# Performance work log

Hardware: AMD Instinct MI355X
Metric: run time of the kernel (lower is better)

## Reference

```python
import jax, jax.numpy as jnp
import numpy as np
from jax import lax

B, L, D, H = 2, 2048, 2048, 16
DH = D // H            # 128 head dim
D_REL = 64             # relevance projection dim (class const)
K = max(1, int(0.25 * L))  # top-K_FRAC tokens per query
NEG_INF = float('-inf')


def setup_inputs() -> dict:
    key = jax.random.key(0)
    ks = jax.random.split(key, 8)
    s = D ** (-0.5)
    return {
        'hidden_states': jax.random.normal(ks[0], (B, L, D), jnp.float32),
        'relevance':     jax.random.normal(ks[1], (B, L, D), jnp.float32),
        # torch nn.Linear weights are [out_features, in_features]
        'W_q_rel': jax.random.normal(ks[2], (D_REL, D), jnp.float32) * s,
        'W_k_rel': jax.random.normal(ks[3], (D_REL, D), jnp.float32) * s,
        'W_q': jax.random.normal(ks[4], (D, D), jnp.float32) * s,
        'W_k': jax.random.normal(ks[5], (D, D), jnp.float32) * s,
        'W_v': jax.random.normal(ks[6], (D, D), jnp.float32) * s,
        'W_o': jax.random.normal(ks[7], (D, D), jnp.float32) * s,
    }


def _rel_scores(relevance, W_q_rel, W_k_rel):
    # low-rank relevance logits, causally masked: [B, L, L]
    q = relevance @ W_q_rel.T   # [B, L, d_rel]
    k = relevance @ W_k_rel.T   # [B, L, d_rel]
    scores = jnp.einsum('bqd,bkd->bqk', q, k) * (D_REL ** -0.5)
    future = jnp.triu(jnp.ones((L, L), dtype=bool), k=1)
    return jnp.where(future[None], NEG_INF, scores)


def _sparse_mask(rel_scores):
    # additive mask [B, 1, L, L]: top-k per query row -> 0.0, else -inf; diag 0.0
    _, topk_idx = lax.top_k(rel_scores, K)            # [B, L, K]
    b = jnp.arange(B)[:, None, None]
    q = jnp.arange(L)[None, :, None]
    mask = jnp.full((B, L, L), NEG_INF, dtype=rel_scores.dtype)
    mask = mask.at[b, q, topk_idx].set(0.0)
    diag = jnp.arange(L)
    mask = mask.at[:, diag, diag].set(0.0)
    return mask[:, None]  # [B, 1, L, L]


def _attention(hidden_states, W_q, W_k, W_v, W_o, add_mask):
    # standard multi-head attention with additive mask (the wrapped frozen attn)
    q = (hidden_states @ W_q.T).reshape(B, L, H, DH)
    k = (hidden_states @ W_k.T).reshape(B, L, H, DH)
    v = (hidden_states @ W_v.T).reshape(B, L, H, DH)
    scores = jnp.einsum('bqhd,bkhd->bhqk', q, k) * (DH ** -0.5)
    scores = scores + add_mask                      # [B, H, L, L]
    p = jax.nn.softmax(scores, axis=-1)
    ctx = jnp.einsum('bhqk,bkhd->bqhd', p, v).reshape(B, L, D)
    return ctx @ W_o.T


def reference(hidden_states, relevance, W_q_rel, W_k_rel, W_q, W_k, W_v, W_o):
    # Phase 1 path (step >= SPARSE_FROM), no external attention_mask:
    # combined = causal(-inf upper-tri) + sparse top-k mask.
    rel = _rel_scores(relevance, W_q_rel, W_k_rel)
    sparse = _sparse_mask(rel)                      # [B, 1, L, L]
    future = jnp.triu(jnp.ones((L, L), dtype=bool), k=1)
    causal = jnp.where(future, NEG_INF, 0.0).astype(hidden_states.dtype)
    combined = causal[None, None] + sparse          # [B, 1, L, L]
    return _attention(hidden_states, W_q, W_k, W_v, W_o, combined)
```

## Files before the change

kernel.cpp:

```cpp
#include <hip/hip_runtime.h>
#include <math.h>
#include <stdint.h>

#define Bb 2
#define Lq 2048
#define Dm 2048
#define Hh 16
#define DH 128
#define DREL 64
#define KTOP 512

#define NEG_INF (-__builtin_huge_valf())

typedef __attribute__((ext_vector_type(8))) short bf16x8;
typedef __attribute__((ext_vector_type(4))) float f32x4;

static __device__ __forceinline__ unsigned short f2bf(float f) {
  unsigned int u = __float_as_uint(f);
  u += 0x7fffu + ((u >> 16) & 1u);
  return (unsigned short)(u >> 16);
}

static __device__ __forceinline__ void gload16(const void* g, void* lds) {
  __builtin_amdgcn_global_load_lds(
      (const __attribute__((address_space(1))) uint32_t*)(uintptr_t)g,
      (__attribute__((address_space(3))) uint32_t*)(uint32_t)(uintptr_t)lds,
      16, 0, 0);
}

__global__ __launch_bounds__(256) void conv_bf16(const float* __restrict__ in,
                                                 unsigned short* __restrict__ out,
                                                 int n8, float scale) {
  const int i = blockIdx.x * 256 + threadIdx.x;
  if (i >= n8) return;
  const float4 f0 = ((const float4*)in)[2 * i];
  const float4 f1 = ((const float4*)in)[2 * i + 1];
  bf16x8 o;
  o[0] = (short)f2bf(f0.x * scale); o[1] = (short)f2bf(f0.y * scale);
  o[2] = (short)f2bf(f0.z * scale); o[3] = (short)f2bf(f0.w * scale);
  o[4] = (short)f2bf(f1.x * scale); o[5] = (short)f2bf(f1.y * scale);
  o[6] = (short)f2bf(f1.z * scale); o[7] = (short)f2bf(f1.w * scale);
  *(bf16x8*)(out + 8 * (size_t)i) = o;
}

__global__ __launch_bounds__(256) void conv_bf16_w4(const float* __restrict__ w0,
                                                    const float* __restrict__ w1,
                                                    const float* __restrict__ w2,
                                                    const float* __restrict__ w3,
                                                    unsigned short* __restrict__ out,
                                                    float s0) {
  const int sel = blockIdx.y;
  const float* in = (sel == 0) ? w0 : (sel == 1) ? w1 : (sel == 2) ? w2 : w3;
  const float scale = (sel == 0) ? s0 : 1.0f;
  const int i = blockIdx.x * 256 + threadIdx.x;
  const float4 f0 = ((const float4*)in)[2 * i];
  const float4 f1 = ((const float4*)in)[2 * i + 1];
  bf16x8 o;
  o[0] = (short)f2bf(f0.x * scale); o[1] = (short)f2bf(f0.y * scale);
  o[2] = (short)f2bf(f0.z * scale); o[3] = (short)f2bf(f0.w * scale);
  o[4] = (short)f2bf(f1.x * scale); o[5] = (short)f2bf(f1.y * scale);
  o[6] = (short)f2bf(f1.z * scale); o[7] = (short)f2bf(f1.w * scale);
  *(bf16x8*)(out + (size_t)sel * Dm * Dm + 8 * (size_t)i) = o;
}

template <bool BF16OUT>
__global__ __launch_bounds__(512, 2) void gemm256(const unsigned short* __restrict__ A,
                                                  const unsigned short* __restrict__ W,
                                                  void* __restrict__ Cv,
                                                  int M, int N, int Kd) {
  __shared__ unsigned short As[2][2][128][64];
  __shared__ unsigned short Bs[2][2][128][64];

  const int tid = threadIdx.x;
  const int w = tid >> 6;
  const int lane = tid & 63;
  const int l15 = lane & 15;
  const int quad = lane >> 4;
  const int wm = w >> 2;
  const int wn = w & 3;

  const int gx = N >> 8;
  const int nwg = (M >> 8) * gx;
  const int cpx = nwg >> 3;
  const int bid = (int)blockIdx.x;
  const int lin = (bid & 7) * cpx + (bid >> 3);
  const int bx = lin % gx, by = lin / gx;
  const int m0 = by * 256, n0 = bx * 256;

  const int srow = lane >> 3;
  const int sslot = (lane & 7) ^ srow;
  const size_t rowK = (size_t)Kd;
  const unsigned short* aG0 = A + (size_t)(m0 + w * 8 + srow) * rowK + sslot * 8;
  const unsigned short* aG1 = aG0 + 64 * rowK;
  const unsigned short* aG2 = aG0 + 128 * rowK;
  const unsigned short* aG3 = aG0 + 192 * rowK;
  const unsigned short* bG0 = W + (size_t)(n0 + w * 8 + srow) * rowK + sslot * 8;
  const unsigned short* bG1 = bG0 + 64 * rowK;
  const unsigned short* bG2 = bG0 + 128 * rowK;
  const unsigned short* bG3 = bG0 + 192 * rowK;

  f32x4 acc[8][4];
#pragma unroll
  for (int i = 0; i < 8; ++i)
#pragma unroll
    for (int j = 0; j < 4; ++j) acc[i][j] = (f32x4){0.f, 0.f, 0.f, 0.f};

  bf16x8 af[4][2];
  bf16x8 bfr[2][2];
  const int swz = (l15 & 7) * 8;

#define STAGE(BUF, T)                                         \
  do {                                                        \
    const size_t ko = (size_t)(T) * 64;                       \
    gload16(aG0 + ko, &As[BUF][0][w * 8][0]);                 \
    gload16(aG1 + ko, &As[BUF][0][64 + w * 8][0]);            \
    gload16(aG2 + ko, &As[BUF][1][w * 8][0]);                 \
    gload16(aG3 + ko, &As[BUF][1][64 + w * 8][0]);            \
    gload16(bG0 + ko, &Bs[BUF][0][w * 8][0]);                 \
    gload16(bG1 + ko, &Bs[BUF][0][64 + w * 8][0]);            \
    gload16(bG2 + ko, &Bs[BUF][1][w * 8][0]);                 \
    gload16(bG3 + ko, &Bs[BUF][1][64 + w * 8][0]);            \
  } while (0)

#define LOAD_A(BUF, MH)                                                        \
  _Pragma("unroll") for (int mi = 0; mi < 4; ++mi)                             \
    _Pragma("unroll") for (int ks = 0; ks < 2; ++ks)                           \
      af[mi][ks] = *(const bf16x8*)&As[BUF][wm][(MH) * 64 + mi * 16 + l15]     \
                                      [(ks * 32 + quad * 8) ^ swz];

#define LOAD_B(BUF, NH)                                                        \
  _Pragma("unroll") for (int ni = 0; ni < 2; ++ni)                             \
    _Pragma("unroll") for (int ks = 0; ks < 2; ++ks)                           \
      bfr[ni][ks] = *(const bf16x8*)&Bs[BUF][wn >> 1]                          \
          [(wn & 1) * 64 + ((NH) * 2 + ni) * 16 + l15]                         \
          [(ks * 32 + quad * 8) ^ swz];

#define PHASE_MFMA(MH, NH)                                                     \
  do {                                                                         \
    __builtin_amdgcn_s_setprio(1);                                             \
    _Pragma("unroll") for (int mi = 0; mi < 4; ++mi)                           \
      _Pragma("unroll") for (int ni = 0; ni < 2; ++ni) {                       \
        acc[(MH) * 4 + mi][(NH) * 2 + ni] =                                    \
            __builtin_amdgcn_mfma_f32_16x16x32_bf16(                           \
                af[mi][0], bfr[ni][0], acc[(MH) * 4 + mi][(NH) * 2 + ni], 0, 0, 0); \
        acc[(MH) * 4 + mi][(NH) * 2 + ni] =                                    \
            __builtin_amdgcn_mfma_f32_16x16x32_bf16(                           \
                af[mi][1], bfr[ni][1], acc[(MH) * 4 + mi][(NH) * 2 + ni], 0, 0, 0); \
      }                                                                        \
    __builtin_amdgcn_s_setprio(0);                                             \
  } while (0)

  STAGE(0, 0);
  __syncthreads();

  const int nt = Kd >> 6;
  int buf = 0;
  for (int t = 0; t < nt; ++t) {
    if (t + 1 < nt) STAGE(buf ^ 1, t + 1);

    LOAD_A(buf, 0);
    LOAD_B(buf, 0);
    PHASE_MFMA(0, 0);
    __builtin_amdgcn_s_barrier();

    LOAD_B(buf, 1);
    PHASE_MFMA(0, 1);
    __builtin_amdgcn_s_barrier();

    LOAD_A(buf, 1);
    PHASE_MFMA(1, 1);
    __builtin_amdgcn_s_barrier();

    LOAD_B(buf, 0);
    PHASE_MFMA(1, 0);

    __syncthreads();
    buf ^= 1;
  }
#undef STAGE
#undef LOAD_A
#undef LOAD_B
#undef PHASE_MFMA

#pragma unroll
  for (int im = 0; im < 8; ++im) {
#pragma unroll
    for (int in = 0; in < 4; ++in) {
      const int col = n0 + wn * 64 + in * 16 + l15;
#pragma unroll
      for (int r = 0; r < 4; ++r) {
        const int row = m0 + wm * 128 + im * 16 + quad * 4 + r;
        if (BF16OUT)
          ((unsigned short*)Cv)[(size_t)row * N + col] = f2bf(acc[im][in][r]);
        else
          ((float*)Cv)[(size_t)row * N + col] = acc[im][in][r];
      }
    }
  }
}

#define RKS 8
__global__ __launch_bounds__(256) void relproj2(const float* __restrict__ A,
                                                const float* __restrict__ Wqr,
                                                const float* __restrict__ Wkr,
                                                float* __restrict__ partq,
                                                float* __restrict__ partk, int M) {
  const float* W = blockIdx.z ? Wkr : Wqr;
  float* part = blockIdx.z ? partk : partq;
  __shared__ float As[16][128];
  __shared__ float Bs[16][64];
  const int ks = blockIdx.x;
  const int m0 = blockIdx.y * 128;
  const int tid = threadIdx.x;
  const int tx = tid & 15;
  const int ty = tid >> 4;
  const int lr = tid >> 1, lk = (tid & 1) * 8;
  const int wr = tid >> 2, wk = (tid & 3) * 4;

  float acc[8][4];
#pragma unroll
  for (int i = 0; i < 8; ++i)
#pragma unroll
    for (int j = 0; j < 4; ++j) acc[i][j] = 0.f;

  const int k00 = ks * (Dm / RKS);
  for (int k0 = k00; k0 < k00 + Dm / RKS; k0 += 16) {
    {
      const float* ap = A + (size_t)(m0 + lr) * Dm + k0 + lk;
      float4 a0 = *(const float4*)(ap);
      float4 a1 = *(const float4*)(ap + 4);
      As[lk + 0][lr] = a0.x; As[lk + 1][lr] = a0.y;
      As[lk + 2][lr] = a0.z; As[lk + 3][lr] = a0.w;
      As[lk + 4][lr] = a1.x; As[lk + 5][lr] = a1.y;
      As[lk + 6][lr] = a1.z; As[lk + 7][lr] = a1.w;
    }
    {
      const float* bp = W + (size_t)wr * Dm + k0 + wk;
      float4 b0 = *(const float4*)(bp);
      Bs[wk + 0][wr] = b0.x; Bs[wk + 1][wr] = b0.y;
      Bs[wk + 2][wr] = b0.z; Bs[wk + 3][wr] = b0.w;
    }
    __syncthreads();
#pragma unroll
    for (int kk = 0; kk < 16; ++kk) {
      float af[8], bf[4];
#pragma unroll
      for (int i = 0; i < 8; ++i) af[i] = As[kk][ty * 8 + i];
#pragma unroll
      for (int j = 0; j < 4; ++j) bf[j] = Bs[kk][tx * 4 + j];
#pragma unroll
      for (int i = 0; i < 8; ++i)
#pragma unroll
        for (int j = 0; j < 4; ++j) acc[i][j] += af[i] * bf[j];
    }
    __syncthreads();
  }

#pragma unroll
  for (int i = 0; i < 8; ++i) {
    float* pp = part + ((size_t)ks * M + m0 + ty * 8 + i) * DREL + tx * 4;
    *(float4*)pp = make_float4(acc[i][0], acc[i][1], acc[i][2], acc[i][3]);
  }
}

__global__ __launch_bounds__(256) void relreduce(const float* __restrict__ pq,
                                                 const float* __restrict__ pk,
                                                 float* __restrict__ qrel,
                                                 float* __restrict__ krel, int n4) {
  const int i = blockIdx.x * 256 + threadIdx.x;
  if (i >= n4) return;
  float4 sq = make_float4(0, 0, 0, 0), sk = sq;
  for (int s = 0; s < RKS; ++s) {
    float4 a = ((const float4*)pq)[(size_t)s * n4 + i];
    float4 b = ((const float4*)pk)[(size_t)s * n4 + i];
    sq.x += a.x; sq.y += a.y; sq.z += a.z; sq.w += a.w;
    sk.x += b.x; sk.y += b.y; sk.z += b.z; sk.w += b.w;
  }
  ((float4*)qrel)[i] = sq;
  ((float4*)krel)[i] = sk;
}

__global__ __launch_bounds__(256) void relscore(const float* __restrict__ qrel,
                                                const float* __restrict__ krel,
                                                float* __restrict__ S) {
  const int jt = blockIdx.x, qt = blockIdx.y, b = blockIdx.z;
  if (jt > qt) return;
  __shared__ float As[16][128];
  __shared__ float Bs[16][128];
  const int tid = threadIdx.x;
  const int q0 = qt * 128, j0 = jt * 128;
  const int tx = tid & 15, ty = tid >> 4;
  const int lr = tid >> 1, lk = (tid & 1) * 8;
  const float* Ab = qrel + (size_t)b * Lq * DREL;
  const float* Kb = krel + (size_t)b * Lq * DREL;

  float acc[8][8];
#pragma unroll
  for (int i = 0; i < 8; ++i)
#pragma unroll
    for (int j = 0; j < 8; ++j) acc[i][j] = 0.f;

  for (int k0 = 0; k0 < DREL; k0 += 16) {
    {
      const float* ap = Ab + (size_t)(q0 + lr) * DREL + k0 + lk;
      float4 a0 = *(const float4*)(ap);
      float4 a1 = *(const float4*)(ap + 4);
      As[lk + 0][lr] = a0.x; As[lk + 1][lr] = a0.y;
      As[lk + 2][lr] = a0.z; As[lk + 3][lr] = a0.w;
      As[lk + 4][lr] = a1.x; As[lk + 5][lr] = a1.y;
      As[lk + 6][lr] = a1.z; As[lk + 7][lr] = a1.w;
    }
    {
      const float* bp = Kb + (size_t)(j0 + lr) * DREL + k0 + lk;
      float4 b0 = *(const float4*)(bp);
      float4 b1 = *(const float4*)(bp + 4);
      Bs[lk + 0][lr] = b0.x; Bs[lk + 1][lr] = b0.y;
      Bs[lk + 2][lr] = b0.z; Bs[lk + 3][lr] = b0.w;
      Bs[lk + 4][lr] = b1.x; Bs[lk + 5][lr] = b1.y;
      Bs[lk + 6][lr] = b1.z; Bs[lk + 7][lr] = b1.w;
    }
    __syncthreads();
#pragma unroll
    for (int kk = 0; kk < 16; ++kk) {
      float af[8], bf[8];
#pragma unroll
      for (int i = 0; i < 8; ++i) af[i] = As[kk][ty * 8 + i];
#pragma unroll
      for (int j = 0; j < 8; ++j) bf[j] = Bs[kk][tx * 8 + j];
#pragma unroll
      for (int i = 0; i < 8; ++i)
#pragma unroll
        for (int j = 0; j < 8; ++j) acc[i][j] += af[i] * bf[j];
    }
    __syncthreads();
  }

  const float sc = 0.125f;
#pragma unroll
  for (int i = 0; i < 8; ++i) {
    float* cp = S + ((size_t)b * Lq + q0 + ty * 8 + i) * Lq + j0 + tx * 8;
    ((float4*)cp)[0] = make_float4(acc[i][0] * sc, acc[i][1] * sc, acc[i][2] * sc, acc[i][3] * sc);
    ((float4*)cp)[1] = make_float4(acc[i][4] * sc, acc[i][5] * sc, acc[i][6] * sc, acc[i][7] * sc);
  }
}

__global__ __launch_bounds__(256) void relselect(const float* __restrict__ S,
                                                 uint32_t* __restrict__ mask) {
  const int w = threadIdx.x >> 6;
  const int lane = threadIdx.x & 63;
  const int ridx = blockIdx.x * 4 + w;
  const int qi = ridx & (Lq - 1);
  const int n = qi + 1;
  const float* srow = S + (size_t)ridx * Lq;

  uint32_t keys[32];
#pragma unroll
  for (int t = 0; t < 32; ++t) {
    const int j = t * 64 + lane;
    const uint32_t u = __float_as_uint(srow[j]);
    const uint32_t k = (u & 0x80000000u) ? ~u : (u | 0x80000000u);
    keys[t] = (j < n) ? k : 0u;
  }

  uint32_t kth = 0u;
  if (n > KTOP) {
    uint32_t pref = 0u;
    int rem = KTOP;
    for (int bit = 31; bit >= 0; --bit) {
      const uint32_t cand = pref | (1u << bit);
      const uint32_t lim = 1u << bit;
      int c = 0;
#pragma unroll
      for (int t = 0; t < 32; ++t) c += ((keys[t] ^ cand) < lim) ? 1 : 0;
      c += __shfl_xor(c, 1);
      c += __shfl_xor(c, 2);
      c += __shfl_xor(c, 4);
      c += __shfl_xor(c, 8);
      c += __shfl_xor(c, 16);
      c += __shfl_xor(c, 32);
      if (c >= rem) pref = cand;
      else rem -= c;
    }
    kth = pref;
  }

  uint32_t* mrow = mask + (size_t)ridx * (Lq / 32);
#pragma unroll
  for (int t = 0; t < 32; ++t) {
    const int j = t * 64 + lane;
    const bool ok = (j < n) && (keys[t] >= kth || j == qi);
    const unsigned long long bal = __ballot(ok);
    if (lane == 0) {
      mrow[2 * t] = (uint32_t)bal;
      mrow[2 * t + 1] = (uint32_t)(bal >> 32);
    }
  }
}

#define ATQ 128
#define TK 64
__global__ __launch_bounds__(512, 4) void attn_flash3(const unsigned short* __restrict__ qkv,
                                                      const uint32_t* __restrict__ mask,
                                                      unsigned short* __restrict__ ctx) {
  __shared__ unsigned short Ks[2][TK][136];
  __shared__ unsigned short Vt[2][2][64][72];
  __shared__ uint32_t mw[2][ATQ][2];

  const int qt = (blockIdx.z == 0) ? ((Lq / ATQ) - 1 - (int)blockIdx.x) : (int)blockIdx.x;
  const int h = blockIdx.y;
  const int b = blockIdx.z;
  const int tid = threadIdx.x;
  const int w = tid >> 6;
  const int lane = tid & 63;
  const int l15 = lane & 15;
  const int quad = lane >> 4;
  const int q0 = qt * ATQ;
  const int STR = 3 * Dm;

  const unsigned short* kbp = qkv + 2048;
  const unsigned short* vbp = qkv + 4096;

  const int myq = q0 + w * 16 + l15;
  const unsigned short* qrow = qkv + (size_t)(b * Lq + myq) * STR + h * DH;
  bf16x8 bq[4];
#pragma unroll
  for (int kk = 0; kk < 4; ++kk) bq[kk] = *(const bf16x8*)(qrow + kk * 32 + quad * 8);

  f32x4 O[8];
#pragma unroll
  for (int f = 0; f < 8; ++f) O[f] = (f32x4){0.f, 0.f, 0.f, 0.f};
  float l_lane = 0.f;

  const int nt = (q0 + ATQ) / TK;

  const int skey = (tid & 255) >> 2;
  const int scg  = tid & 3;
  const int mq   = (tid & 255) >> 1;
  const int msel = tid & 1;
  const int tv = tid - 256;
  const int vkp = tv & 31;
  const int vdg = (tv >> 5) & 7;
  const int vhalf = vkp >> 4;
  const int vkp16 = vkp & 15;
  const int dwc = ((vkp16 >> 1) & 3) * 4 + (vkp16 >> 3) * 2 + (vkp16 & 1);

  const uint32_t* mrow_base = mask + (size_t)(b * Lq + q0 + mq) * (Lq / 32) + msel;
  const unsigned short* krow_base = kbp + (size_t)(b * Lq + skey) * STR + h * DH + scg * 32;
  const unsigned short* vrow_base = vbp + (size_t)(b * Lq + 2 * vkp) * STR + h * DH + vdg * 16;

  bf16x8 r0, r1, r2, r3;
  uint32_t mreg = 0;

#define LOADREGS(KT)                                                       \
  do {                                                                     \
    const int kbase_ = (KT) * TK;                                          \
    if (tid < 256) {                                                       \
      const unsigned short* kr = krow_base + (size_t)kbase_ * STR;         \
      r0 = *(const bf16x8*)(kr);                                           \
      r1 = *(const bf16x8*)(kr + 8);                                       \
      r2 = *(const bf16x8*)(kr + 16);                                      \
      r3 = *(const bf16x8*)(kr + 24);                                      \
      mreg = mrow_base[(KT) * 2];                                          \
    } else {                                                               \
      const unsigned short* vr = vrow_base + (size_t)kbase_ * STR;         \
      r0 = *(const bf16x8*)(vr);                                           \
      r1 = *(const bf16x8*)(vr + 8);                                       \
      r2 = *(const bf16x8*)(vr + STR);                                     \
      r3 = *(const bf16x8*)(vr + STR + 8);                                 \
    }                                                                      \
  } while (0)

#define WRITELDS(BUF)                                                      \
  do {                                                                     \
    if (tid < 256) {                                                       \
      *(bf16x8*)&Ks[BUF][skey][scg * 32 + 0]  = r0;                        \
      *(bf16x8*)&Ks[BUF][skey][scg * 32 + 8]  = r1;                        \
      *(bf16x8*)&Ks[BUF][skey][scg * 32 + 16] = r2;                        \
      *(bf16x8*)&Ks[BUF][skey][scg * 32 + 24] = r3;                        \
      mw[BUF][mq][msel] = mreg;                                            \
    } else {                                                               \
      _Pragma("unroll") for (int i = 0; i < 8; ++i) {                      \
        const int d = vdg * 16 + i;                                        \
        const uint32_t pk = (uint32_t)(unsigned short)r0[i] |              \
                            ((uint32_t)(unsigned short)r2[i] << 16);       \
        ((uint32_t*)&Vt[BUF][vhalf][d >> 1][0])[(d & 1) * 16 + dwc] = pk;  \
      }                                                                    \
      _Pragma("unroll") for (int i = 0; i < 8; ++i) {                      \
        const int d = vdg * 16 + 8 + i;                                    \
        const uint32_t pk = (uint32_t)(unsigned short)r1[i] |              \
                            ((uint32_t)(unsigned short)r3[i] << 16);       \
        ((uint32_t*)&Vt[BUF][vhalf][d >> 1][0])[(d & 1) * 16 + dwc] = pk;  \
      }                                                                    \
    }                                                                      \
  } while (0)

  LOADREGS(0);
  WRITELDS(0);
  __syncthreads();

  int buf = 0;
  for (int kt = 0; kt < nt; ++kt) {
    const bool more = (kt + 1 < nt);
    if (more) LOADREGS(kt + 1);

    __builtin_amdgcn_s_setprio(1);
#pragma unroll
    for (int hh = 0; hh < 2; ++hh) {
      f32x4 acc0 = (f32x4){0.f, 0.f, 0.f, 0.f};
      f32x4 acc1 = acc0;
#pragma unroll
      for (int kk = 0; kk < 4; ++kk) {
        bf16x8 a0 = *(const bf16x8*)&Ks[buf][hh * 32 + l15][kk * 32 + quad * 8];
        bf16x8 a1 = *(const bf16x8*)&Ks[buf][hh * 32 + 16 + l15][kk * 32 + quad * 8];
        acc0 = __builtin_amdgcn_mfma_f32_16x16x32_bf16(a0, bq[kk], acc0, 0, 0, 0);
        acc1 = __builtin_amdgcn_mfma_f32_16x16x32_bf16(a1, bq[kk], acc1, 0, 0, 0);
      }

      const uint32_t mword = mw[buf][w * 16 + l15][hh];
      bf16x8 bp;
      float ps = 0.f;
#pragma unroll
      for (int r = 0; r < 4; ++r) {
        const float p0 = ((mword >> (quad * 4 + r)) & 1u) ? __builtin_amdgcn_exp2f(acc0[r]) : 0.f;
        const float p1 = ((mword >> (16 + quad * 4 + r)) & 1u) ? __builtin_amdgcn_exp2f(acc1[r]) : 0.f;
        ps += p0 + p1;
        bp[r] = (short)f2bf(p0);
        bp[4 + r] = (short)f2bf(p1);
      }
      l_lane += ps;

#pragma unroll
      for (int f = 0; f < 8; ++f) {
        const int d = f * 16 + l15;
        bf16x8 av = *(const bf16x8*)&Vt[buf][hh][d >> 1][(d & 1) * 32 + quad * 8];
        O[f] = __builtin_amdgcn_mfma_f32_16x16x32_bf16(av, bp, O[f], 0, 0, 0);
      }
    }
    __builtin_amdgcn_s_setprio(0);

    if (more) WRITELDS(buf ^ 1);
    __syncthreads();
    buf ^= 1;
  }
#undef LOADREGS
#undef WRITELDS

  l_lane += __shfl_xor(l_lane, 16);
  l_lane += __shfl_xor(l_lane, 32);
  const float rl = 1.0f / l_lane;

  unsigned short* orow = ctx + ((size_t)(b * Lq + q0 + w * 16 + l15)) * Dm + h * DH;
#pragma unroll
  for (int f = 0; f < 8; ++f) {
    ushort4 o4;
    o4.x = f2bf(O[f][0] * rl);
    o4.y = f2bf(O[f][1] * rl);
    o4.z = f2bf(O[f][2] * rl);
    o4.w = f2bf(O[f][3] * rl);
    *(ushort4*)(orow + f * 16 + quad * 4) = o4;
  }
}

extern "C" void kernel_launch(void* const* d_in, const int* in_sizes, int n_in,
                              void* d_out, int out_size, void* d_ws, size_t ws_size,
                              hipStream_t stream) {
  const float* hs  = (const float*)d_in[0];
  const float* rel = (const float*)d_in[1];
  const float* Wqr = (const float*)d_in[2];
  const float* Wkr = (const float*)d_in[3];
  const float* Wq  = (const float*)d_in[4];
  const float* Wk  = (const float*)d_in[5];
  const float* Wv  = (const float*)d_in[6];
  const float* Wo  = (const float*)d_in[7];
  float* out = (float*)d_out;

  const int M = Bb * Lq;
  const int ND = Dm * Dm;
  char* ws = (char*)d_ws;
  size_t off = 0;
  float* qrel = (float*)(ws + off); off += (size_t)M * DREL * 4;
  float* krel = (float*)(ws + off); off += (size_t)M * DREL * 4;
  uint32_t* maskb = (uint32_t*)(ws + off); off += (size_t)M * (Lq / 32) * 4;
  float* partq = (float*)(ws + off); off += (size_t)RKS * M * DREL * 4;
  float* partk = (float*)(ws + off); off += (size_t)RKS * M * DREL * 4;
  float* Sbuf = (float*)(ws + off);
  unsigned short* hsb  = (unsigned short*)(ws + off); off += (size_t)M * Dm * 2;
  unsigned short* qkvb = (unsigned short*)(ws + off); off += (size_t)M * 3 * Dm * 2;
  unsigned short* ctxb = (unsigned short*)(ws + off); off += (size_t)M * Dm * 2;
  unsigned short* Wqkvo = (unsigned short*)(ws + off); off += (size_t)4 * ND * 2;

  const dim3 blk(256);
  const int hsN8 = M * Dm / 8;
  const float QSCALE = 0.08838834764831845f * 1.4426950408889634f;

  relproj2<<<dim3(RKS, M / 128, 2), blk, 0, stream>>>(rel, Wqr, Wkr, partq, partk, M);
  relreduce<<<(M * DREL / 4 + 255) / 256, blk, 0, stream>>>(partq, partk, qrel, krel, M * DREL / 4);
  relscore<<<dim3(Lq / 128, Lq / 128, Bb), blk, 0, stream>>>(qrel, krel, Sbuf);
  relselect<<<M / 4, blk, 0, stream>>>(Sbuf, maskb);

  conv_bf16<<<(hsN8 + 255) / 256, blk, 0, stream>>>(hs, hsb, hsN8, 1.0f);
  conv_bf16_w4<<<dim3(ND / 8 / 256, 4), blk, 0, stream>>>(Wq, Wk, Wv, Wo, Wqkvo, QSCALE);

  gemm256<true><<<dim3((M / 256) * (3 * Dm / 256)), dim3(512), 0, stream>>>(
      hsb, Wqkvo, qkvb, M, 3 * Dm, Dm);

  attn_flash3<<<dim3(Lq / ATQ, Hh, Bb), dim3(512), 0, stream>>>(qkvb, maskb, ctxb);

  gemm256<false><<<dim3((M / 256) * (Dm / 256)), dim3(512), 0, stream>>>(
      ctxb, Wqkvo + (size_t)3 * ND, out, M, Dm, Dm);
}
```

Measured before the change: 489.8 us.

## Restructure GEMM mainloop into half-K sub-stage pipeline with finer global-to-LDS prefetch

Splits each 64-wide K tile in LDS into two 32-wide halves and interleaves global-to-LDS loads for future tiles (t+1, t+2) between MFMA phases, gated by explicit vmcnt waits and raw s_barriers instead of a full syncthreads per iteration. It also changes the LDS swizzle and staging mapping, and switches the block raster order to walk M-first. The aim is to hide global load latency better and cut per-iteration barrier stalls in the projection GEMMs. In exchange it relies on hand-counted vmcnt values and buffer reuse within an iteration, which is fragile and can introduce races if a count is off.

```diff
diff --git a/kernel.cpp b/kernel.cpp
--- a/kernel.cpp
+++ b/kernel.cpp
@@ -68,8 +68,8 @@
                                                   const unsigned short* __restrict__ W,
                                                   void* __restrict__ Cv,
                                                   int M, int N, int Kd) {
-  __shared__ unsigned short As[2][2][128][64];
-  __shared__ unsigned short Bs[2][2][128][64];
+  __shared__ unsigned short As[2][2][2][128][32];
+  __shared__ unsigned short Bs[2][2][2][128][32];
 
   const int tid = threadIdx.x;
   const int w = tid >> 6;
@@ -79,25 +79,19 @@
   const int wm = w >> 2;
   const int wn = w & 3;
 
-  const int gx = N >> 8;
-  const int nwg = (M >> 8) * gx;
+  const int gy = M >> 8;
+  const int nwg = gy * (N >> 8);
   const int cpx = nwg >> 3;
   const int bid = (int)blockIdx.x;
   const int lin = (bid & 7) * cpx + (bid >> 3);
-  const int bx = lin % gx, by = lin / gx;
+  const int by = lin % gy, bx = lin / gy;
   const int m0 = by * 256, n0 = bx * 256;
 
-  const int srow = lane >> 3;
-  const int sslot = (lane & 7) ^ srow;
-  const size_t rowK = (size_t)Kd;
-  const unsigned short* aG0 = A + (size_t)(m0 + w * 8 + srow) * rowK + sslot * 8;
-  const unsigned short* aG1 = aG0 + 64 * rowK;
-  const unsigned short* aG2 = aG0 + 128 * rowK;
-  const unsigned short* aG3 = aG0 + 192 * rowK;
-  const unsigned short* bG0 = W + (size_t)(n0 + w * 8 + srow) * rowK + sslot * 8;
-  const unsigned short* bG1 = bG0 + 64 * rowK;
-  const unsigned short* bG2 = bG0 + 128 * rowK;
-  const unsigned short* bG3 = bG0 + 192 * rowK;
+  const int srow = w * 16 + (lane >> 2);
+  const int sslot = (lane & 3) ^ ((lane >> 3) & 3);
+  const unsigned short* aB = A + (size_t)(m0 + srow) * Kd + sslot * 8;
+  const unsigned short* bB = W + (size_t)(n0 + srow) * Kd + sslot * 8;
+  const size_t hstep = (size_t)128 * Kd;
 
   f32x4 acc[8][4];
 #pragma unroll
@@ -105,82 +99,93 @@
 #pragma unroll
     for (int j = 0; j < 4; ++j) acc[i][j] = (f32x4){0.f, 0.f, 0.f, 0.f};
 
-  bf16x8 af[4][2];
-  bf16x8 bfr[2][2];
-  const int swz = (l15 & 7) * 8;
-
-#define STAGE(BUF, T)                                         \
-  do {                                                        \
-    const size_t ko = (size_t)(T) * 64;                       \
-    gload16(aG0 + ko, &As[BUF][0][w * 8][0]);                 \
-    gload16(aG1 + ko, &As[BUF][0][64 + w * 8][0]);            \
-    gload16(aG2 + ko, &As[BUF][1][w * 8][0]);                 \
-    gload16(aG3 + ko, &As[BUF][1][64 + w * 8][0]);            \
-    gload16(bG0 + ko, &Bs[BUF][0][w * 8][0]);                 \
-    gload16(bG1 + ko, &Bs[BUF][0][64 + w * 8][0]);            \
-    gload16(bG2 + ko, &Bs[BUF][1][w * 8][0]);                 \
-    gload16(bG3 + ko, &Bs[BUF][1][64 + w * 8][0]);            \
+  bf16x8 af[8], bfr[2];
+  const int rswz = (quad ^ ((l15 >> 1) & 3)) * 8;
+
+#define ST_A(BUF, S, T)                                                     \
+  do {                                                                      \
+    const size_t ko = (size_t)(T) * 64 + (S) * 32;                          \
+    gload16(aB + ko, &As[BUF][0][S][w * 16][0]);                            \
+    gload16(aB + hstep + ko, &As[BUF][1][S][w * 16][0]);                    \
   } while (0)
 
-#define LOAD_A(BUF, MH)                                                        \
-  _Pragma("unroll") for (int mi = 0; mi < 4; ++mi)                             \
-    _Pragma("unroll") for (int ks = 0; ks < 2; ++ks)                           \
-      af[mi][ks] = *(const bf16x8*)&As[BUF][wm][(MH) * 64 + mi * 16 + l15]     \
-                                      [(ks * 32 + quad * 8) ^ swz];
-
-#define LOAD_B(BUF, NH)                                                        \
-  _Pragma("unroll") for (int ni = 0; ni < 2; ++ni)                             \
-    _Pragma("unroll") for (int ks = 0; ks < 2; ++ks)                           \
-      bfr[ni][ks] = *(const bf16x8*)&Bs[BUF][wn >> 1]                          \
-          [(wn & 1) * 64 + ((NH) * 2 + ni) * 16 + l15]                         \
-          [(ks * 32 + quad * 8) ^ swz];
-
-#define PHASE_MFMA(MH, NH)                                                     \
-  do {                                                                         \
-    __builtin_amdgcn_s_setprio(1);                                             \
-    _Pragma("unroll") for (int mi = 0; mi < 4; ++mi)                           \
-      _Pragma("unroll") for (int ni = 0; ni < 2; ++ni) {                       \
-        acc[(MH) * 4 + mi][(NH) * 2 + ni] =                                    \
-            __builtin_amdgcn_mfma_f32_16x16x32_bf16(                           \
-                af[mi][0], bfr[ni][0], acc[(MH) * 4 + mi][(NH) * 2 + ni], 0, 0, 0); \
-        acc[(MH) * 4 + mi][(NH) * 2 + ni] =                                    \
-            __builtin_amdgcn_mfma_f32_16x16x32_bf16(                           \
-                af[mi][1], bfr[ni][1], acc[(MH) * 4 + mi][(NH) * 2 + ni], 0, 0, 0); \
-      }                                                                        \
-    __builtin_amdgcn_s_setprio(0);                                             \
+#define ST_B(BUF, S, T)                                                     \
+  do {                                                                      \
+    const size_t ko = (size_t)(T) * 64 + (S) * 32;                          \
+    gload16(bB + ko, &Bs[BUF][0][S][w * 16][0]);                            \
+    gload16(bB + hstep + ko, &Bs[BUF][1][S][w * 16][0]);                    \
   } while (0)
 
-  STAGE(0, 0);
-  __syncthreads();
+#define LD_A(BUF, S)                                                        \
+  _Pragma("unroll") for (int mi = 0; mi < 8; ++mi)                          \
+      af[mi] = *(const bf16x8*)&As[BUF][wm][S][mi * 16 + l15][rswz];
+
+#define LD_B(BUF, S, NP)                                                    \
+  _Pragma("unroll") for (int ni = 0; ni < 2; ++ni)                          \
+      bfr[ni] = *(const bf16x8*)&Bs[BUF][wn >> 1][S]                        \
+          [(wn & 1) * 64 + ((NP) * 2 + ni) * 16 + l15][rswz];
+
+#define MFMA16(NP)                                                          \
+  do {                                                                      \
+    __builtin_amdgcn_s_setprio(1);                                          \
+    _Pragma("unroll") for (int mi = 0; mi < 8; ++mi)                        \
+        _Pragma("unroll") for (int ni = 0; ni < 2; ++ni)                    \
+            acc[mi][(NP) * 2 + ni] = __builtin_amdgcn_mfma_f32_16x16x32_bf16( \
+                af[mi], bfr[ni], acc[mi][(NP) * 2 + ni], 0, 0, 0);          \
+    __builtin_amdgcn_s_setprio(0);                                          \
+  } while (0)
+
+#define SBAR()        asm volatile("s_barrier" ::: "memory")
+#define WAITBAR(N)    asm volatile("s_waitcnt vmcnt(" #N ")\ns_barrier" ::: "memory")
+
+  ST_A(0, 0, 0); ST_B(0, 0, 0); ST_A(0, 1, 0); ST_B(0, 1, 0);
+  ST_A(1, 0, 1); ST_B(1, 0, 1); ST_A(1, 1, 1);
+  WAITBAR(6);
 
   const int nt = Kd >> 6;
   int buf = 0;
-  for (int t = 0; t < nt; ++t) {
-    if (t + 1 < nt) STAGE(buf ^ 1, t + 1);
-
-    LOAD_A(buf, 0);
-    LOAD_B(buf, 0);
-    PHASE_MFMA(0, 0);
-    __builtin_amdgcn_s_barrier();
-
-    LOAD_B(buf, 1);
-    PHASE_MFMA(0, 1);
-    __builtin_amdgcn_s_barrier();
-
-    LOAD_A(buf, 1);
-    PHASE_MFMA(1, 1);
-    __builtin_amdgcn_s_barrier();
-
-    LOAD_B(buf, 0);
-    PHASE_MFMA(1, 0);
-
-    __syncthreads();
+  for (int t = 0; t < nt - 2; ++t) {
+    LD_A(buf, 0);
+    LD_B(buf, 0, 0);
+    ST_B(buf ^ 1, 1, t + 1);
+    SBAR();
+    MFMA16(0);
+    SBAR();
+    LD_B(buf, 0, 1);
+    ST_A(buf, 0, t + 2);
+    WAITBAR(10);
+    MFMA16(1);
+    SBAR();
+    LD_A(buf, 1);
+    LD_B(buf, 1, 0);
+    ST_B(buf, 0, t + 2);
+    SBAR();
+    MFMA16(0);
+    SBAR();
+    LD_B(buf, 1, 1);
+    ST_A(buf, 1, t + 2);
+    WAITBAR(10);
+    MFMA16(1);
+    SBAR();
     buf ^= 1;
   }
-#undef STAGE
-#undef LOAD_A
-#undef LOAD_B
-#undef PHASE_MFMA
+
+  ST_B(buf ^ 1, 1, nt - 1);
+  WAITBAR(0);
+  for (int g = 0; g < 2; ++g) {
+    LD_A(buf, 0); LD_B(buf, 0, 0); MFMA16(0);
+    LD_B(buf, 0, 1);               MFMA16(1);
+    LD_A(buf, 1); LD_B(buf, 1, 0); MFMA16(0);
+    LD_B(buf, 1, 1);               MFMA16(1);
+    buf ^= 1;
+  }
+#undef ST_A
+#undef ST_B
+#undef LD_A
+#undef LD_B
+#undef MFMA16
+#undef SBAR
+#undef WAITBAR
 
 #pragma unroll
   for (int im = 0; im < 8; ++im) {
```

Result: no change. 482.7 us (-1.4%).
